# Optimization experiments

Measured on AMD Instinct MI355X. Metric: run time of the kernel, lower is better.

Reference implementation:

```python
import jax, jax.numpy as jnp
import numpy as np

B, S, D, O = 1024, 200, 512, 512


def setup_inputs() -> dict:
    key = jax.random.key(0)
    ks = jax.random.split(key, 8)
    x = jax.random.normal(ks[0], (B, S, D), dtype=jnp.float32)
    # prefix mask: sqlen in [2, S] so keys slice [:sqlen-1] is non-empty
    sqlen = jax.random.randint(ks[1], (B,), 2, S + 1)
    mask = (jnp.arange(S)[None, :] < sqlen[:, None]).astype(jnp.int32)
    lim = 1.0 / np.sqrt(D)
    Wq_w = jax.random.uniform(ks[2], (O, D), minval=-lim, maxval=lim)
    Wk_w = jax.random.uniform(ks[3], (O, D), minval=-lim, maxval=lim)
    Wv_w = jax.random.uniform(ks[4], (O, D), minval=-lim, maxval=lim)
    Wq_b = jax.random.uniform(ks[5], (O,), minval=-lim, maxval=lim)
    Wk_b = jax.random.uniform(ks[6], (O,), minval=-lim, maxval=lim)
    Wv_b = jax.random.uniform(ks[7], (O,), minval=-lim, maxval=lim)
    return {"input": x, "mask": mask, "Wq_w": Wq_w, "Wq_b": Wq_b,
            "Wk_w": Wk_w, "Wk_b": Wk_b, "Wv_w": Wv_w, "Wv_b": Wv_b}


def reference(input, mask, Wq_w, Wq_b, Wk_w, Wk_b, Wv_w, Wv_b):
    b, s, d = input.shape
    sqlen = jnp.sum(mask, axis=1).astype(jnp.int32)          # [B]
    # query = last valid token; keys/values = tokens [0, sqlen-1)
    last = input[jnp.arange(b), sqlen - 1]                   # [B, D]
    q = last @ Wq_w.T + Wq_b                                 # [B, O]
    K = jnp.einsum('bsd,od->bso', input, Wk_w) + Wk_b        # [B, S, O]
    V = jnp.einsum('bsd,od->bso', input, Wv_w) + Wv_b        # [B, S, O]
    scores = jnp.einsum('bo,bso->bs', q, K)                  # no 1/sqrt(d), faithful
    valid = jnp.arange(s)[None, :] < (sqlen - 1)[:, None]    # [B, S]
    scores = jnp.where(valid, scores, -jnp.inf)
    attn = jax.nn.softmax(scores, axis=-1)
    out = jnp.einsum('bs,bso->bo', attn, V)                  # [B, O]
    # dropout p=0.5 treated as identity (eval mode / deterministic reference)
    return jnp.tanh(out)
```

## Files before the change

kernel.cpp:

```cpp
#include <hip/hip_runtime.h>
#include <hip/hip_bf16.h>
#include <math.h>

#define B_  1024
#define S_  200
#define D_  512
#define O_  512

__global__ __launch_bounds__(64) void prep_kernel(
    const float* __restrict__ x, const int* __restrict__ mask,
    int* __restrict__ sqlen, float* __restrict__ last)
{
    const int b = blockIdx.x;
    const int lane = threadIdx.x;

    int ssum = 0;
    for (int i = lane; i < S_; i += 64) ssum += mask[b * S_ + i];
#pragma unroll
    for (int off = 32; off; off >>= 1) ssum += __shfl_xor(ssum, off);

    if (lane == 0) sqlen[b] = ssum;

    const float* row = x + ((size_t)b * S_ + (ssum - 1)) * D_;
    float4 v0 = *(const float4*)(row + lane * 8);
    float4 v1 = *(const float4*)(row + lane * 8 + 4);
    *(float4*)(last + (size_t)b * D_ + lane * 8)     = v0;
    *(float4*)(last + (size_t)b * D_ + lane * 8 + 4) = v1;
}

template<int AMODE, int BMODE, bool BIASOUT, bool BIAS, bool TANH>
__global__ __launch_bounds__(64) void gemm16(
    const float* __restrict__ A, const float* __restrict__ Bm,
    const float* __restrict__ bias, float* __restrict__ C,
    float* __restrict__ cvec, const float* __restrict__ bfold,
    int M, int N, int K, int lda, int ldb)
{
    constexpr int SA = (AMODE == 0) ? 22 : 20;
    constexpr int SB = (BMODE == 0) ? 22 : 20;
    __shared__ float As[32 * SA];
    __shared__ float Bs[32 * SB];
    __shared__ float sBq[32];

    const int lane = threadIdx.x;
    const int m0 = blockIdx.x * 16;
    const int n0 = blockIdx.y * 16;
    const int ly = lane >> 3;
    const int lx = lane & 7;

    float a00 = 0.f, a01 = 0.f, a10 = 0.f, a11 = 0.f;
    float cb0 = 0.f, cb1 = 0.f;

    for (int k0 = 0; k0 < K; k0 += 32) {
        float4 av0, av1, bv0, bv1;
        if (AMODE == 0) {
            const float* p = A + (size_t)(m0 + (lane >> 2)) * lda + k0 + ((lane & 3) << 3);
            av0 = *(const float4*)p;  av1 = *(const float4*)(p + 4);
        } else {
            const float* p = A + (size_t)(k0 + (lane >> 1)) * lda + m0 + ((lane & 1) << 3);
            av0 = *(const float4*)p;  av1 = *(const float4*)(p + 4);
        }
        if (BMODE == 0) {
            const float* p = Bm + (size_t)(n0 + (lane >> 2)) * ldb + k0 + ((lane & 3) << 3);
            bv0 = *(const float4*)p;  bv1 = *(const float4*)(p + 4);
        } else {
            const float* p = Bm + (size_t)(k0 + (lane >> 1)) * ldb + n0 + ((lane & 1) << 3);
            bv0 = *(const float4*)p;  bv1 = *(const float4*)(p + 4);
        }
        float bqv = 0.f;
        if (BIASOUT) bqv = bfold[k0 + (lane & 31)];

        __syncthreads();

        if (AMODE == 0) {
            const int mr = lane >> 2, kc = (lane & 3) << 3;
            As[(kc + 0) * SA + mr] = av0.x; As[(kc + 1) * SA + mr] = av0.y;
            As[(kc + 2) * SA + mr] = av0.z; As[(kc + 3) * SA + mr] = av0.w;
            As[(kc + 4) * SA + mr] = av1.x; As[(kc + 5) * SA + mr] = av1.y;
            As[(kc + 6) * SA + mr] = av1.z; As[(kc + 7) * SA + mr] = av1.w;
        } else {
            const int kr = lane >> 1, mc = (lane & 1) << 3;
            *(float4*)&As[kr * SA + mc]     = av0;
            *(float4*)&As[kr * SA + mc + 4] = av1;
        }
        if (BMODE == 0) {
            const int nr = lane >> 2, kc = (lane & 3) << 3;
            Bs[(kc + 0) * SB + nr] = bv0.x; Bs[(kc + 1) * SB + nr] = bv0.y;
            Bs[(kc + 2) * SB + nr] = bv0.z; Bs[(kc + 3) * SB + nr] = bv0.w;
            Bs[(kc + 4) * SB + nr] = bv1.x; Bs[(kc + 5) * SB + nr] = bv1.y;
            Bs[(kc + 6) * SB + nr] = bv1.z; Bs[(kc + 7) * SB + nr] = bv1.w;
        } else {
            const int kr = lane >> 1, nc = (lane & 1) << 3;
            *(float4*)&Bs[kr * SB + nc]     = bv0;
            *(float4*)&Bs[kr * SB + nc + 4] = bv1;
        }
        if (BIASOUT && lane < 32) sBq[lane] = bqv;

        __syncthreads();

#pragma unroll
        for (int kk = 0; kk < 32; ++kk) {
            float2 a = *(const float2*)&As[kk * SA + (ly << 1)];
            float2 b = *(const float2*)&Bs[kk * SB + (lx << 1)];
            a00 = fmaf(a.x, b.x, a00); a01 = fmaf(a.x, b.y, a01);
            a10 = fmaf(a.y, b.x, a10); a11 = fmaf(a.y, b.y, a11);
            if (BIASOUT) {
                float qv = sBq[kk];
                cb0 = fmaf(qv, b.x, cb0); cb1 = fmaf(qv, b.y, cb1);
            }
        }
    }

    const int r0 = m0 + (ly << 1);
    const int c0 = n0 + (lx << 1);
    float o00 = a00, o01 = a01, o10 = a10, o11 = a11;
    if (BIAS) {
        float b0 = bias[c0], b1 = bias[c0 + 1];
        o00 += b0; o01 += b1; o10 += b0; o11 += b1;
    }
    if (TANH) { o00 = tanhf(o00); o01 = tanhf(o01); o10 = tanhf(o10); o11 = tanhf(o11); }
    *(float2*)(C + (size_t)r0 * N + c0)       = make_float2(o00, o01);
    *(float2*)(C + (size_t)(r0 + 1) * N + c0) = make_float2(o10, o11);

    if (BIASOUT && blockIdx.x == 0 && ly == 0)
        *(float2*)(cvec + c0) = make_float2(cb0, cb1);
}

__global__ __launch_bounds__(256) void attn_kernel(
    const float* __restrict__ x, const float* __restrict__ qk,
    const int* __restrict__ sqlen, float* __restrict__ ctx)
{
    const int b    = blockIdx.x;
    const int tid  = threadIdx.x;
    const int w    = tid >> 6;
    const int lane = tid & 63;
    const int L    = sqlen[b] - 1;

    const float* qkb = qk + (size_t)b * D_ + lane * 8;
    const float4 q0 = *(const float4*)qkb;
    const float4 q1 = *(const float4*)(qkb + 4);

    float m = -INFINITY, l = 0.f;
    float acc[8] = {0.f, 0.f, 0.f, 0.f, 0.f, 0.f, 0.f, 0.f};

    int s0 = w * 2;
    if (s0 < L) {
        const float* base = x + (size_t)b * S_ * D_ + lane * 8;
        const int s1c = (s0 + 1 < L) ? s0 + 1 : s0;
        float4 c0 = *(const float4*)(base + (size_t)s0  * D_);
        float4 c1 = *(const float4*)(base + (size_t)s0  * D_ + 4);
        float4 c2 = *(const float4*)(base + (size_t)s1c * D_);
        float4 c3 = *(const float4*)(base + (size_t)s1c * D_ + 4);
        for (;;) {
            const int  sn   = s0 + 8;
            const bool more = sn < L;
            const int  sp0  = more ? sn : s0;
            const int  sp1  = (sn + 1 < L) ? sn + 1 : sp0;
            float4 n0 = *(const float4*)(base + (size_t)sp0 * D_);
            float4 n1 = *(const float4*)(base + (size_t)sp0 * D_ + 4);
            float4 n2 = *(const float4*)(base + (size_t)sp1 * D_);
            float4 n3 = *(const float4*)(base + (size_t)sp1 * D_ + 4);

            float p0 = c0.x*q0.x + c0.y*q0.y + c0.z*q0.z + c0.w*q0.w
                     + c1.x*q1.x + c1.y*q1.y + c1.z*q1.z + c1.w*q1.w;
            float p1 = c2.x*q0.x + c2.y*q0.y + c2.z*q0.z + c2.w*q0.w
                     + c3.x*q1.x + c3.y*q1.y + c3.z*q1.z + c3.w*q1.w;
#pragma unroll
            for (int off = 32; off; off >>= 1) {
                p0 += __shfl_xor(p0, off);
                p1 += __shfl_xor(p1, off);
            }
            if (s0 + 1 >= L) p1 = -INFINITY;

            const float mn = fmaxf(m, fmaxf(p0, p1));
            const float r  = __expf(m  - mn);
            const float e0 = __expf(p0 - mn);
            const float e1 = __expf(p1 - mn);
            l = l * r + e0 + e1;
            acc[0] = acc[0]*r + e0*c0.x + e1*c2.x;
            acc[1] = acc[1]*r + e0*c0.y + e1*c2.y;
            acc[2] = acc[2]*r + e0*c0.z + e1*c2.z;
            acc[3] = acc[3]*r + e0*c0.w + e1*c2.w;
            acc[4] = acc[4]*r + e0*c1.x + e1*c3.x;
            acc[5] = acc[5]*r + e0*c1.y + e1*c3.y;
            acc[6] = acc[6]*r + e0*c1.z + e1*c3.z;
            acc[7] = acc[7]*r + e0*c1.w + e1*c3.w;
            m = mn;

            if (!more) break;
            s0 = sn; c0 = n0; c1 = n1; c2 = n2; c3 = n3;
        }
    }

    __shared__ float s_m[4], s_l[4];
    __shared__ float s_ctx[4][D_];
    if (lane == 0) { s_m[w] = m; s_l[w] = l; }
#pragma unroll
    for (int j = 0; j < 8; ++j) s_ctx[w][lane * 8 + j] = acc[j];
    __syncthreads();

    const float M4 = fmaxf(fmaxf(s_m[0], s_m[1]), fmaxf(s_m[2], s_m[3]));
    const float sc0 = __expf(s_m[0] - M4);
    const float sc1 = __expf(s_m[1] - M4);
    const float sc2 = __expf(s_m[2] - M4);
    const float sc3 = __expf(s_m[3] - M4);
    const float lt  = s_l[0]*sc0 + s_l[1]*sc1 + s_l[2]*sc2 + s_l[3]*sc3;
    const float inv = 1.f / lt;

    const int d = tid * 2;
    float v0 = (s_ctx[0][d]     * sc0 + s_ctx[1][d]     * sc1 +
                s_ctx[2][d]     * sc2 + s_ctx[3][d]     * sc3) * inv;
    float v1 = (s_ctx[0][d + 1] * sc0 + s_ctx[1][d + 1] * sc1 +
                s_ctx[2][d + 1] * sc2 + s_ctx[3][d + 1] * sc3) * inv;
    *(float2*)(ctx + (size_t)b * D_ + d) = make_float2(v0, v1);
}

extern "C" void kernel_launch(void* const* d_in, const int* in_sizes, int n_in,
                              void* d_out, int out_size, void* d_ws, size_t ws_size,
                              hipStream_t stream)
{
    const float* x    = (const float*)d_in[0];
    const int*   mask = (const int*)  d_in[1];
    const float* Wq_w = (const float*)d_in[2];
    const float* Wq_b = (const float*)d_in[3];
    const float* Wk_w = (const float*)d_in[4];
    const float* Wk_b = (const float*)d_in[5];
    const float* Wv_w = (const float*)d_in[6];
    const float* Wv_b = (const float*)d_in[7];
    (void)Wk_b; (void)in_sizes; (void)n_in; (void)out_size; (void)ws_size;
    float* out = (float*)d_out;

    char* ws = (char*)d_ws;
    int*   sqlen = (int*)ws;
    float* cvec  = (float*)(ws + 4096);
    float* Wqk   = (float*)(ws + 8192);
    float* last  = (float*)(ws + 8192 + (1u << 20));
    float* qk    = last + (size_t)B_ * D_;
    float* ctxb  = qk   + (size_t)B_ * D_;

    gemm16<1, 1, true, false, false><<<dim3(32, 32), 64, 0, stream>>>(
        Wq_w, Wk_w, nullptr, Wqk, cvec, Wq_b, D_, D_, O_, D_, D_);

    prep_kernel<<<B_, 64, 0, stream>>>(x, mask, sqlen, last);

    gemm16<0, 1, false, true, false><<<dim3(B_ / 16, D_ / 16), 64, 0, stream>>>(
        last, Wqk, cvec, qk, nullptr, nullptr, B_, D_, D_, D_, D_);

    attn_kernel<<<B_, 256, 0, stream>>>(x, qk, sqlen, ctxb);

    gemm16<0, 0, false, true, true><<<dim3(B_ / 16, O_ / 16), 64, 0, stream>>>(
        ctxb, Wv_w, Wv_b, out, nullptr, nullptr, B_, O_, D_, D_, D_);
}
```

Baseline: 592.4 us.

## Fuse setup kernels, gather last row in GEMM, widen GEMM and attention tiles

The Wq·Wk fold GEMM and the mask-length reduction now run in a single launch, using block-index partitioning. The separate copy of the last token is removed because the qk GEMM gathers rows directly from x. Both GEMMs use 32x16 tiles instead of 16x16, which raises per-thread reuse. The attention kernel processes four rows per wave per step instead of two. Together these cut launches and intermediate traffic and add memory-level parallelism, at the cost of more registers and fewer GEMM blocks.

After: 593.4 us. No clear change (+0.2%).

```diff
diff --git a/kernel.cpp b/kernel.cpp
--- a/kernel.cpp
+++ b/kernel.cpp
@@ -7,94 +7,50 @@
 #define D_  512
 #define O_  512
 
-__global__ __launch_bounds__(64) void prep_kernel(
-    const float* __restrict__ x, const int* __restrict__ mask,
-    int* __restrict__ sqlen, float* __restrict__ last)
+__global__ __launch_bounds__(64) void setup_kernel(
+    const float* __restrict__ Wq_w, const float* __restrict__ Wk_w,
+    const float* __restrict__ Wq_b, const int* __restrict__ mask,
+    float* __restrict__ Wqk, float* __restrict__ cvec, int* __restrict__ sqlen)
 {
-    const int b = blockIdx.x;
+    const int bid  = blockIdx.x;
     const int lane = threadIdx.x;
 
-    int ssum = 0;
-    for (int i = lane; i < S_; i += 64) ssum += mask[b * S_ + i];
-#pragma unroll
-    for (int off = 32; off; off >>= 1) ssum += __shfl_xor(ssum, off);
-
-    if (lane == 0) sqlen[b] = ssum;
-
-    const float* row = x + ((size_t)b * S_ + (ssum - 1)) * D_;
-    float4 v0 = *(const float4*)(row + lane * 8);
-    float4 v1 = *(const float4*)(row + lane * 8 + 4);
-    *(float4*)(last + (size_t)b * D_ + lane * 8)     = v0;
-    *(float4*)(last + (size_t)b * D_ + lane * 8 + 4) = v1;
-}
-
-template<int AMODE, int BMODE, bool BIASOUT, bool BIAS, bool TANH>
-__global__ __launch_bounds__(64) void gemm16(
-    const float* __restrict__ A, const float* __restrict__ Bm,
-    const float* __restrict__ bias, float* __restrict__ C,
-    float* __restrict__ cvec, const float* __restrict__ bfold,
-    int M, int N, int K, int lda, int ldb)
-{
-    constexpr int SA = (AMODE == 0) ? 22 : 20;
-    constexpr int SB = (BMODE == 0) ? 22 : 20;
+    if (bid >= 1024) {
+        const int b = bid - 1024;
+        int ssum = 0;
+        for (int i = lane; i < S_; i += 64) ssum += mask[b * S_ + i];
+#pragma unroll
+        for (int off = 32; off; off >>= 1) ssum += __shfl_xor(ssum, off);
+        if (lane == 0) sqlen[b] = ssum;
+        return;
+    }
+
+    constexpr int SA = 20, SB = 20;
     __shared__ float As[32 * SA];
     __shared__ float Bs[32 * SB];
     __shared__ float sBq[32];
 
-    const int lane = threadIdx.x;
-    const int m0 = blockIdx.x * 16;
-    const int n0 = blockIdx.y * 16;
-    const int ly = lane >> 3;
-    const int lx = lane & 7;
+    const int m0 = (bid & 31) * 16;
+    const int n0 = (bid >> 5) * 16;
+    const int ly = lane >> 3, lx = lane & 7;
+    const int kr = lane >> 1, c8 = (lane & 1) << 3;
 
     float a00 = 0.f, a01 = 0.f, a10 = 0.f, a11 = 0.f;
     float cb0 = 0.f, cb1 = 0.f;
 
-    for (int k0 = 0; k0 < K; k0 += 32) {
-        float4 av0, av1, bv0, bv1;
-        if (AMODE == 0) {
-            const float* p = A + (size_t)(m0 + (lane >> 2)) * lda + k0 + ((lane & 3) << 3);
-            av0 = *(const float4*)p;  av1 = *(const float4*)(p + 4);
-        } else {
-            const float* p = A + (size_t)(k0 + (lane >> 1)) * lda + m0 + ((lane & 1) << 3);
-            av0 = *(const float4*)p;  av1 = *(const float4*)(p + 4);
-        }
-        if (BMODE == 0) {
-            const float* p = Bm + (size_t)(n0 + (lane >> 2)) * ldb + k0 + ((lane & 3) << 3);
-            bv0 = *(const float4*)p;  bv1 = *(const float4*)(p + 4);
-        } else {
-            const float* p = Bm + (size_t)(k0 + (lane >> 1)) * ldb + n0 + ((lane & 1) << 3);
-            bv0 = *(const float4*)p;  bv1 = *(const float4*)(p + 4);
-        }
-        float bqv = 0.f;
-        if (BIASOUT) bqv = bfold[k0 + (lane & 31)];
+    for (int k0 = 0; k0 < O_; k0 += 32) {
+        const float* pa = Wq_w + (size_t)(k0 + kr) * D_ + m0 + c8;
+        float4 av0 = *(const float4*)pa, av1 = *(const float4*)(pa + 4);
+        const float* pb = Wk_w + (size_t)(k0 + kr) * D_ + n0 + c8;
+        float4 bv0 = *(const float4*)pb, bv1 = *(const float4*)(pb + 4);
+        float bqv = Wq_b[k0 + (lane & 31)];
 
         __syncthreads();
-
-        if (AMODE == 0) {
-            const int mr = lane >> 2, kc = (lane & 3) << 3;
-            As[(kc + 0) * SA + mr] = av0.x; As[(kc + 1) * SA + mr] = av0.y;
-            As[(kc + 2) * SA + mr] = av0.z; As[(kc + 3) * SA + mr] = av0.w;
-            As[(kc + 4) * SA + mr] = av1.x; As[(kc + 5) * SA + mr] = av1.y;
-            As[(kc + 6) * SA + mr] = av1.z; As[(kc + 7) * SA + mr] = av1.w;
-        } else {
-            const int kr = lane >> 1, mc = (lane & 1) << 3;
-            *(float4*)&As[kr * SA + mc]     = av0;
-            *(float4*)&As[kr * SA + mc + 4] = av1;
-        }
-        if (BMODE == 0) {
-            const int nr = lane >> 2, kc = (lane & 3) << 3;
-            Bs[(kc + 0) * SB + nr] = bv0.x; Bs[(kc + 1) * SB + nr] = bv0.y;
-            Bs[(kc + 2) * SB + nr] = bv0.z; Bs[(kc + 3) * SB + nr] = bv0.w;
-            Bs[(kc + 4) * SB + nr] = bv1.x; Bs[(kc + 5) * SB + nr] = bv1.y;
-            Bs[(kc + 6) * SB + nr] = bv1.z; Bs[(kc + 7) * SB + nr] = bv1.w;
-        } else {
-            const int kr = lane >> 1, nc = (lane & 1) << 3;
-            *(float4*)&Bs[kr * SB + nc]     = bv0;
-            *(float4*)&Bs[kr * SB + nc + 4] = bv1;
-        }
-        if (BIASOUT && lane < 32) sBq[lane] = bqv;
-
+        *(float4*)&As[kr * SA + c8]     = av0;
+        *(float4*)&As[kr * SA + c8 + 4] = av1;
+        *(float4*)&Bs[kr * SB + c8]     = bv0;
+        *(float4*)&Bs[kr * SB + c8 + 4] = bv1;
+        if (lane < 32) sBq[lane] = bqv;
         __syncthreads();
 
 #pragma unroll
@@ -103,26 +59,109 @@
             float2 b = *(const float2*)&Bs[kk * SB + (lx << 1)];
             a00 = fmaf(a.x, b.x, a00); a01 = fmaf(a.x, b.y, a01);
             a10 = fmaf(a.y, b.x, a10); a11 = fmaf(a.y, b.y, a11);
-            if (BIASOUT) {
-                float qv = sBq[kk];
-                cb0 = fmaf(qv, b.x, cb0); cb1 = fmaf(qv, b.y, cb1);
-            }
+            float qv = sBq[kk];
+            cb0 = fmaf(qv, b.x, cb0); cb1 = fmaf(qv, b.y, cb1);
         }
     }
 
     const int r0 = m0 + (ly << 1);
     const int c0 = n0 + (lx << 1);
-    float o00 = a00, o01 = a01, o10 = a10, o11 = a11;
-    if (BIAS) {
-        float b0 = bias[c0], b1 = bias[c0 + 1];
-        o00 += b0; o01 += b1; o10 += b0; o11 += b1;
-    }
-    if (TANH) { o00 = tanhf(o00); o01 = tanhf(o01); o10 = tanhf(o10); o11 = tanhf(o11); }
-    *(float2*)(C + (size_t)r0 * N + c0)       = make_float2(o00, o01);
-    *(float2*)(C + (size_t)(r0 + 1) * N + c0) = make_float2(o10, o11);
-
-    if (BIASOUT && blockIdx.x == 0 && ly == 0)
+    *(float2*)(Wqk + (size_t)r0 * D_ + c0)       = make_float2(a00, a01);
+    *(float2*)(Wqk + (size_t)(r0 + 1) * D_ + c0) = make_float2(a10, a11);
+    if ((bid & 31) == 0 && ly == 0)
         *(float2*)(cvec + c0) = make_float2(cb0, cb1);
+}
+
+template<bool GATHER, int BMODE, bool TANH>
+__global__ __launch_bounds__(64) void gemm32x16(
+    const float* __restrict__ A, const float* __restrict__ Bm,
+    const float* __restrict__ bias, float* __restrict__ C,
+    const int* __restrict__ sq, int N, int K, int lda, int ldb)
+{
+    constexpr int SA = 34;
+    constexpr int SB = (BMODE == 0) ? 18 : 20;
+    __shared__ float As[32 * SA];
+    __shared__ float Bs[32 * SB];
+
+    const int lane = threadIdx.x;
+    const int m0 = blockIdx.x * 32;
+    const int n0 = blockIdx.y * 16;
+    const int ly = lane >> 3, lx = lane & 7;
+
+    const int ar  = lane >> 1;
+    const int akc = (lane & 1) << 4;
+    const float* arow;
+    if (GATHER) {
+        const int b = m0 + ar;
+        arow = A + ((size_t)b * S_ + (sq[b] - 1)) * (size_t)lda + akc;
+    } else {
+        arow = A + (size_t)(m0 + ar) * lda + akc;
+    }
+
+    float l00 = 0.f, l01 = 0.f, l10 = 0.f, l11 = 0.f;
+    float h00 = 0.f, h01 = 0.f, h10 = 0.f, h11 = 0.f;
+
+    for (int k0 = 0; k0 < K; k0 += 32) {
+        float4 a0 = *(const float4*)(arow + k0);
+        float4 a1 = *(const float4*)(arow + k0 + 4);
+        float4 a2 = *(const float4*)(arow + k0 + 8);
+        float4 a3 = *(const float4*)(arow + k0 + 12);
+        float4 b0, b1;
+        if (BMODE == 1) {
+            const float* pb = Bm + (size_t)(k0 + (lane >> 1)) * ldb + n0 + ((lane & 1) << 3);
+            b0 = *(const float4*)pb; b1 = *(const float4*)(pb + 4);
+        } else {
+            const float* pb = Bm + (size_t)(n0 + (lane >> 2)) * ldb + k0 + ((lane & 3) << 3);
+            b0 = *(const float4*)pb; b1 = *(const float4*)(pb + 4);
+        }
+
+        __syncthreads();
+
+        {
+            const float av[16] = {a0.x,a0.y,a0.z,a0.w, a1.x,a1.y,a1.z,a1.w,
+                                  a2.x,a2.y,a2.z,a2.w, a3.x,a3.y,a3.z,a3.w};
+#pragma unroll
+            for (int j = 0; j < 16; ++j) As[(akc + j) * SA + ar] = av[j];
+        }
+        if (BMODE == 1) {
+            const int kr = lane >> 1, nc = (lane & 1) << 3;
+            *(float4*)&Bs[kr * SB + nc]     = b0;
+            *(float4*)&Bs[kr * SB + nc + 4] = b1;
+        } else {
+            const int nr = lane >> 2, kc = (lane & 3) << 3;
+            Bs[(kc + 0) * SB + nr] = b0.x; Bs[(kc + 1) * SB + nr] = b0.y;
+            Bs[(kc + 2) * SB + nr] = b0.z; Bs[(kc + 3) * SB + nr] = b0.w;
+            Bs[(kc + 4) * SB + nr] = b1.x; Bs[(kc + 5) * SB + nr] = b1.y;
+            Bs[(kc + 6) * SB + nr] = b1.z; Bs[(kc + 7) * SB + nr] = b1.w;
+        }
+        __syncthreads();
+
+#pragma unroll
+        for (int kk = 0; kk < 32; ++kk) {
+            float2 al = *(const float2*)&As[kk * SA + (ly << 1)];
+            float2 ah = *(const float2*)&As[kk * SA + 16 + (ly << 1)];
+            float2 b  = *(const float2*)&Bs[kk * SB + (lx << 1)];
+            l00 = fmaf(al.x, b.x, l00); l01 = fmaf(al.x, b.y, l01);
+            l10 = fmaf(al.y, b.x, l10); l11 = fmaf(al.y, b.y, l11);
+            h00 = fmaf(ah.x, b.x, h00); h01 = fmaf(ah.x, b.y, h01);
+            h10 = fmaf(ah.y, b.x, h10); h11 = fmaf(ah.y, b.y, h11);
+        }
+    }
+
+    const int c0 = n0 + (lx << 1);
+    const float bb0 = bias[c0], bb1 = bias[c0 + 1];
+    float o0 = l00 + bb0, o1 = l01 + bb1, o2 = l10 + bb0, o3 = l11 + bb1;
+    float o4 = h00 + bb0, o5 = h01 + bb1, o6 = h10 + bb0, o7 = h11 + bb1;
+    if (TANH) {
+        o0 = tanhf(o0); o1 = tanhf(o1); o2 = tanhf(o2); o3 = tanhf(o3);
+        o4 = tanhf(o4); o5 = tanhf(o5); o6 = tanhf(o6); o7 = tanhf(o7);
+    }
+    const int rl = m0 + (ly << 1);
+    const int rh = rl + 16;
+    *(float2*)(C + (size_t)rl * N + c0)       = make_float2(o0, o1);
+    *(float2*)(C + (size_t)(rl + 1) * N + c0) = make_float2(o2, o3);
+    *(float2*)(C + (size_t)rh * N + c0)       = make_float2(o4, o5);
+    *(float2*)(C + (size_t)(rh + 1) * N + c0) = make_float2(o6, o7);
 }
 
 __global__ __launch_bounds__(256) void attn_kernel(
@@ -142,52 +181,76 @@
     float m = -INFINITY, l = 0.f;
     float acc[8] = {0.f, 0.f, 0.f, 0.f, 0.f, 0.f, 0.f, 0.f};
 
-    int s0 = w * 2;
+    int s0 = w * 4;
     if (s0 < L) {
         const float* base = x + (size_t)b * S_ * D_ + lane * 8;
-        const int s1c = (s0 + 1 < L) ? s0 + 1 : s0;
-        float4 c0 = *(const float4*)(base + (size_t)s0  * D_);
-        float4 c1 = *(const float4*)(base + (size_t)s0  * D_ + 4);
-        float4 c2 = *(const float4*)(base + (size_t)s1c * D_);
-        float4 c3 = *(const float4*)(base + (size_t)s1c * D_ + 4);
+        const int i1 = (s0 + 1 < L) ? s0 + 1 : L - 1;
+        const int i2 = (s0 + 2 < L) ? s0 + 2 : L - 1;
+        const int i3 = (s0 + 3 < L) ? s0 + 3 : L - 1;
+        float4 c0 = *(const float4*)(base + (size_t)s0 * D_);
+        float4 c1 = *(const float4*)(base + (size_t)s0 * D_ + 4);
+        float4 c2 = *(const float4*)(base + (size_t)i1 * D_);
+        float4 c3 = *(const float4*)(base + (size_t)i1 * D_ + 4);
+        float4 c4 = *(const float4*)(base + (size_t)i2 * D_);
+        float4 c5 = *(const float4*)(base + (size_t)i2 * D_ + 4);
+        float4 c6 = *(const float4*)(base + (size_t)i3 * D_);
+        float4 c7 = *(const float4*)(base + (size_t)i3 * D_ + 4);
         for (;;) {
-            const int  sn   = s0 + 8;
+            const int  sn   = s0 + 16;
             const bool more = sn < L;
-            const int  sp0  = more ? sn : s0;
-            const int  sp1  = (sn + 1 < L) ? sn + 1 : sp0;
-            float4 n0 = *(const float4*)(base + (size_t)sp0 * D_);
-            float4 n1 = *(const float4*)(base + (size_t)sp0 * D_ + 4);
-            float4 n2 = *(const float4*)(base + (size_t)sp1 * D_);
-            float4 n3 = *(const float4*)(base + (size_t)sp1 * D_ + 4);
+            const int  j0 = more ? sn : s0;
+            const int  j1 = more ? ((sn + 1 < L) ? sn + 1 : L - 1) : s0;
+            const int  j2 = more ? ((sn + 2 < L) ? sn + 2 : L - 1) : s0;
+            const int  j3 = more ? ((sn + 3 < L) ? sn + 3 : L - 1) : s0;
+            float4 n0 = *(const float4*)(base + (size_t)j0 * D_);
+            float4 n1 = *(const float4*)(base + (size_t)j0 * D_ + 4);
+            float4 n2 = *(const float4*)(base + (size_t)j1 * D_);
+            float4 n3 = *(const float4*)(base + (size_t)j1 * D_ + 4);
+            float4 n4 = *(const float4*)(base + (size_t)j2 * D_);
+            float4 n5 = *(const float4*)(base + (size_t)j2 * D_ + 4);
+            float4 n6 = *(const float4*)(base + (size_t)j3 * D_);
+            float4 n7 = *(const float4*)(base + (size_t)j3 * D_ + 4);
 
             float p0 = c0.x*q0.x + c0.y*q0.y + c0.z*q0.z + c0.w*q0.w
                      + c1.x*q1.x + c1.y*q1.y + c1.z*q1.z + c1.w*q1.w;
             float p1 = c2.x*q0.x + c2.y*q0.y + c2.z*q0.z + c2.w*q0.w
                      + c3.x*q1.x + c3.y*q1.y + c3.z*q1.z + c3.w*q1.w;
+            float p2 = c4.x*q0.x + c4.y*q0.y + c4.z*q0.z + c4.w*q0.w
+                     + c5.x*q1.x + c5.y*q1.y + c5.z*q1.z + c5.w*q1.w;
+            float p3 = c6.x*q0.x + c6.y*q0.y + c6.z*q0.z + c6.w*q0.w
+                     + c7.x*q1.x + c7.y*q1.y + c7.z*q1.z + c7.w*q1.w;
 #pragma unroll
             for (int off = 32; off; off >>= 1) {
                 p0 += __shfl_xor(p0, off);
                 p1 += __shfl_xor(p1, off);
+                p2 += __shfl_xor(p2, off);
+                p3 += __shfl_xor(p3, off);
             }
             if (s0 + 1 >= L) p1 = -INFINITY;
-
-            const float mn = fmaxf(m, fmaxf(p0, p1));
+            if (s0 + 2 >= L) p2 = -INFINITY;
+            if (s0 + 3 >= L) p3 = -INFINITY;
+
+            const float mn = fmaxf(fmaxf(m, fmaxf(p0, p1)), fmaxf(p2, p3));
             const float r  = __expf(m  - mn);
             const float e0 = __expf(p0 - mn);
             const float e1 = __expf(p1 - mn);
-            l = l * r + e0 + e1;
-            acc[0] = acc[0]*r + e0*c0.x + e1*c2.x;
-            acc[1] = acc[1]*r + e0*c0.y + e1*c2.y;
-            acc[2] = acc[2]*r + e0*c0.z + e1*c2.z;
-            acc[3] = acc[3]*r + e0*c0.w + e1*c2.w;
-            acc[4] = acc[4]*r + e0*c1.x + e1*c3.x;
-            acc[5] = acc[5]*r + e0*c1.y + e1*c3.y;
-            acc[6] = acc[6]*r + e0*c1.z + e1*c3.z;
-            acc[7] = acc[7]*r + e0*c1.w + e1*c3.w;
+            const float e2 = __expf(p2 - mn);
+            const float e3 = __expf(p3 - mn);
+            l = l * r + e0 + e1 + e2 + e3;
+            acc[0] = acc[0]*r + e0*c0.x + e1*c2.x + e2*c4.x + e3*c6.x;
+            acc[1] = acc[1]*r + e0*c0.y + e1*c2.y + e2*c4.y + e3*c6.y;
+            acc[2] = acc[2]*r + e0*c0.z + e1*c2.z + e2*c4.z + e3*c6.z;
+            acc[3] = acc[3]*r + e0*c0.w + e1*c2.w + e2*c4.w + e3*c6.w;
+            acc[4] = acc[4]*r + e0*c1.x + e1*c3.x + e2*c5.x + e3*c7.x;
+            acc[5] = acc[5]*r + e0*c1.y + e1*c3.y + e2*c5.y + e3*c7.y;
+            acc[6] = acc[6]*r + e0*c1.z + e1*c3.z + e2*c5.z + e3*c7.z;
+            acc[7] = acc[7]*r + e0*c1.w + e1*c3.w + e2*c5.w + e3*c7.w;
             m = mn;
 
             if (!more) break;
-            s0 = sn; c0 = n0; c1 = n1; c2 = n2; c3 = n3;
+            s0 = sn;
+            c0 = n0; c1 = n1; c2 = n2; c3 = n3;
+            c4 = n4; c5 = n5; c6 = n6; c7 = n7;
         }
     }
 
@@ -233,20 +296,16 @@
     int*   sqlen = (int*)ws;
     float* cvec  = (float*)(ws + 4096);
     float* Wqk   = (float*)(ws + 8192);
-    float* last  = (float*)(ws + 8192 + (1u << 20));
-    float* qk    = last + (size_t)B_ * D_;
-    float* ctxb  = qk   + (size_t)B_ * D_;
-
-    gemm16<1, 1, true, false, false><<<dim3(32, 32), 64, 0, stream>>>(
-        Wq_w, Wk_w, nullptr, Wqk, cvec, Wq_b, D_, D_, O_, D_, D_);
-
-    prep_kernel<<<B_, 64, 0, stream>>>(x, mask, sqlen, last);
-
-    gemm16<0, 1, false, true, false><<<dim3(B_ / 16, D_ / 16), 64, 0, stream>>>(
-        last, Wqk, cvec, qk, nullptr, nullptr, B_, D_, D_, D_, D_);
+    float* qk    = (float*)(ws + 8192 + (1u << 20));
+    float* ctxb  = qk + (size_t)B_ * D_;
+
+    setup_kernel<<<2048, 64, 0, stream>>>(Wq_w, Wk_w, Wq_b, mask, Wqk, cvec, sqlen);
+
+    gemm32x16<true, 1, false><<<dim3(B_ / 32, D_ / 16), 64, 0, stream>>>(
+        x, Wqk, cvec, qk, sqlen, D_, D_, D_, D_);
 
     attn_kernel<<<B_, 256, 0, stream>>>(x, qk, sqlen, ctxb);
 
-    gemm16<0, 0, false, true, true><<<dim3(B_ / 16, O_ / 16), 64, 0, stream>>>(
-        ctxb, Wv_w, Wv_b, out, nullptr, nullptr, B_, O_, D_, D_, D_);
+    gemm32x16<false, 0, true><<<dim3(B_ / 32, O_ / 16), 64, 0, stream>>>(
+        ctxb, Wv_w, Wv_b, out, nullptr, O_, D_, D_, D_);
 }
```
